# Optimization experiments

Hardware: AMD Instinct MI355X
Metric: run time of the kernel (lower is better)

Reference implementation:

```python
import jax, jax.numpy as jnp
import numpy as np

N_NODES = 50000
NEG_SLOPE = 0.2


def setup_inputs() -> dict:
    key = jax.random.key(0)
    k1, k2, k3, k4, k5 = jax.random.split(key, 5)
    in_c, out_c = 256, 256
    n_edges = 1_600_000
    x = jax.random.normal(k1, (N_NODES, in_c), dtype=jnp.float32)
    edge_index = jax.random.randint(k2, (2, n_edges), 0, N_NODES, dtype=jnp.int64)
    # Glorot-ish scaled params
    W = jax.random.normal(k3, (in_c, out_c), dtype=jnp.float32) * (1.0 / np.sqrt(in_c))
    att_src = jax.random.normal(k4, (out_c,), dtype=jnp.float32) * (1.0 / np.sqrt(out_c))
    att_dst = jax.random.normal(k5, (out_c,), dtype=jnp.float32) * (1.0 / np.sqrt(out_c))
    bias = jnp.zeros((out_c,), dtype=jnp.float32)
    return {"x": x, "edge_index": edge_index, "W": W, "att_src": att_src, "att_dst": att_dst, "bias": bias}


def reference(x, edge_index, W, att_src, att_dst, bias):
    N = x.shape[0]
    # PyG GATConv default: add self loops
    loops = jnp.arange(N, dtype=edge_index.dtype)
    src = jnp.concatenate([edge_index[0], loops])  # [E+N]
    dst = jnp.concatenate([edge_index[1], loops])  # [E+N]

    h = x @ W  # [N, out_c]
    a_s = h @ att_src  # [N] per-node source attention term
    a_d = h @ att_dst  # [N] per-node destination attention term

    e = a_s[src] + a_d[dst]  # [E+N]
    e = jnp.where(e > 0, e, NEG_SLOPE * e)  # LeakyReLU(0.2)

    # scatter-softmax over edges sharing a destination node
    e_max = jax.ops.segment_max(e, dst, num_segments=N)  # [N]
    e_exp = jnp.exp(e - e_max[dst])  # [E+N]
    denom = jax.ops.segment_sum(e_exp, dst, num_segments=N)  # [N]
    alpha = e_exp / denom[dst]  # [E+N]

    msgs = alpha[:, None] * h[src]  # [E+N, out_c]
    out = jax.ops.segment_sum(msgs, dst, num_segments=N)  # [N, out_c]
    return out + bias
```

## Files before the change

kernel.cpp:

```cpp
#include <hip/hip_runtime.h>
#include <math.h>

#define NODES_C 256
#define NEG_SLOPE 0.2f
#define CAP 128
#define NSLICE 8

typedef __attribute__((ext_vector_type(8))) short short8;
typedef __attribute__((ext_vector_type(4))) float f32x4;
typedef __attribute__((ext_vector_type(2))) float f32x2;
typedef __attribute__((ext_vector_type(4))) int i32x4;

__device__ inline unsigned short f2bf(float f) {
    unsigned u = __float_as_uint(f);
    u = (u + 0x7fff + ((u >> 16) & 1)) >> 16;
    return (unsigned short)u;
}
__device__ inline unsigned cvtpk_bf16(float a, float b) {
    unsigned r;
    asm("v_cvt_pk_bf16_f32 %0, %1, %2" : "=v"(r) : "v"(a), "v"(b));
    return r;
}
__device__ inline void gload_lds16(const void* g, void* l) {
    __builtin_amdgcn_global_load_lds(
        (const __attribute__((address_space(1))) unsigned int*)g,
        (__attribute__((address_space(3))) unsigned int*)l, 16, 0, 0);
}
__device__ inline void fma2(f32x2& a, unsigned u, float w) {
    f32x2 h;
    h.x = __uint_as_float(u << 16);
    h.y = __uint_as_float(u & 0xffff0000u);
    a += h * w;
}

__global__ __launch_bounds__(256) void k_init(const float* __restrict__ W,
                                              unsigned short* __restrict__ wt,
                                              uint4* __restrict__ zbase,
                                              int nZero4, int nbZero) {
    const int tid = threadIdx.x;
    int bid = blockIdx.x;
    if (bid < nbZero) {
        const int base = bid * 1024 + tid;
#pragma unroll
        for (int k = 0; k < 4; ++k) {
            const int i = base + k * 256;
            if (i < nZero4) zbase[i] = make_uint4(0, 0, 0, 0);
        }
        return;
    }
    bid -= nbZero;
    const int base = bid * 1024 + tid;
#pragma unroll
    for (int k = 0; k < 4; ++k) {
        const int i = base + k * 256;
        wt[i] = f2bf(W[(i & 255) * NODES_C + (i >> 8)]);
    }
}

__global__ __launch_bounds__(256) void k_stageB(
    const float* __restrict__ x, const unsigned short* __restrict__ wt,
    const float* __restrict__ att_src, const float* __restrict__ att_dst,
    unsigned short* __restrict__ hb, float* __restrict__ a_s, float* __restrict__ a_d,
    int n) {
    __shared__ unsigned short Ab[128 * 32];
    __shared__ unsigned short Bb[128 * 32];
    __shared__ float pfs[2][128], pfd[2][128];
    const int tid = threadIdx.x;
    const int lane = tid & 63;
    const int wid = tid >> 6;

    const int gbid = blockIdx.x;
    const int wr = wid >> 1, wc = wid & 1;
    const int brow = (gbid >> 1) * 128;
    const int bcol = (gbid & 1) * 128;
    const int rsel = lane & 15, ksel = (lane >> 4) * 8;

    f32x4 acc[4][4] = {};
    const int c0 = wid, c1 = wid + 4;
    const int srow0 = c0 * 16 + (lane >> 2), srow1 = c1 * 16 + (lane >> 2);
    const int sk = (lane & 3) * 8;
    const int arow = tid >> 1;
    const int kh = (tid & 1) * 16;
    const float4* xsrc = (const float4*)(x + (size_t)min(brow + arow, n - 1) * NODES_C);
    uint4* adst = (uint4*)&Ab[arow * 32 + kh];

    for (int kk = 0; kk < 256; kk += 32) {
        const int kb = (kk + kh) >> 2;
        const float4 v0 = xsrc[kb + 0];
        const float4 v1 = xsrc[kb + 1];
        const float4 v2 = xsrc[kb + 2];
        const float4 v3 = xsrc[kb + 3];
        gload_lds16(wt + (size_t)(bcol + srow0) * NODES_C + kk + sk, Bb + c0 * 512);
        gload_lds16(wt + (size_t)(bcol + srow1) * NODES_C + kk + sk, Bb + c1 * 512);
        adst[0] = make_uint4(cvtpk_bf16(v0.x, v0.y), cvtpk_bf16(v0.z, v0.w),
                             cvtpk_bf16(v1.x, v1.y), cvtpk_bf16(v1.z, v1.w));
        adst[1] = make_uint4(cvtpk_bf16(v2.x, v2.y), cvtpk_bf16(v2.z, v2.w),
                             cvtpk_bf16(v3.x, v3.y), cvtpk_bf16(v3.z, v3.w));
        __syncthreads();
        short8 afrag[4], bfrag[4];
#pragma unroll
        for (int m = 0; m < 4; ++m)
            afrag[m] = *(const short8*)&Ab[(wr * 64 + m * 16 + rsel) * 32 + ksel];
#pragma unroll
        for (int q = 0; q < 4; ++q)
            bfrag[q] = *(const short8*)&Bb[(wc * 64 + q * 16 + rsel) * 32 + ksel];
#pragma unroll
        for (int m = 0; m < 4; ++m)
#pragma unroll
            for (int q = 0; q < 4; ++q)
                acc[m][q] = __builtin_amdgcn_mfma_f32_16x16x32_bf16(bfrag[q], afrag[m], acc[m][q], 0, 0, 0);
        __syncthreads();
    }

    const int xr = lane & 15;
    const int cg = (lane >> 4) * 4;
    float4 avs4[4], avd4[4];
#pragma unroll
    for (int q = 0; q < 4; ++q) {
        avs4[q] = *(const float4*)&att_src[bcol + wc * 64 + q * 16 + cg];
        avd4[q] = *(const float4*)&att_dst[bcol + wc * 64 + q * 16 + cg];
    }
#pragma unroll
    for (int m = 0; m < 4; ++m) {
        const int rloc = wr * 64 + m * 16 + xr;
        const int r = brow + rloc;
        float s = 0.f, d = 0.f;
#pragma unroll
        for (int q = 0; q < 4; ++q) {
            const f32x4 v = acc[m][q];
            s += v[0] * avs4[q].x + v[1] * avs4[q].y + v[2] * avs4[q].z + v[3] * avs4[q].w;
            d += v[0] * avd4[q].x + v[1] * avd4[q].y + v[2] * avd4[q].z + v[3] * avd4[q].w;
            if (r < n) {
                const uint2 hv = make_uint2(cvtpk_bf16(v[0], v[1]), cvtpk_bf16(v[2], v[3]));
                *(uint2*)&hb[(size_t)r * NODES_C + bcol + wc * 64 + q * 16 + cg] = hv;
            }
        }
        s += __shfl_xor(s, 16); s += __shfl_xor(s, 32);
        d += __shfl_xor(d, 16); d += __shfl_xor(d, 32);
        if (lane < 16) { pfs[wc][rloc] = s; pfd[wc][rloc] = d; }
    }
    __syncthreads();
    if (tid < 128) {
        const int r = brow + tid;
        if (r < n) atomicAdd(&a_s[r], pfs[0][tid] + pfs[1][tid]);
    } else {
        const int t2 = tid - 128;
        const int r = brow + t2;
        if (r < n) atomicAdd(&a_d[r], pfd[0][t2] + pfd[1][t2]);
    }
}

__global__ __launch_bounds__(256) void k_permute(const int* __restrict__ src,
                                                 const int* __restrict__ dst,
                                                 const float* __restrict__ a_s,
                                                 const float* __restrict__ a_d,
                                                 int* __restrict__ cnt,
                                                 unsigned* __restrict__ sedge,
                                                 int E4, int bps, int nsNode, int n) {
    const int slice = blockIdx.x & (NSLICE - 1);
    const int j = blockIdx.x >> 3;
    const int lo = slice * nsNode;
    const int hi = min(lo + nsNode, n);
    const int stride = bps * 256;
    const i32x4* d4 = (const i32x4*)dst;
    const i32x4* s4 = (const i32x4*)src;

    for (int g = j * 256 + threadIdx.x; g < E4; g += stride) {
        const i32x4 dv = __builtin_nontemporal_load(&d4[g]);
        const bool m0 = (dv.x >= lo) & (dv.x < hi);
        const bool m1 = (dv.y >= lo) & (dv.y < hi);
        const bool m2 = (dv.z >= lo) & (dv.z < hi);
        const bool m3 = (dv.w >= lo) & (dv.w < hi);
        if (!(m0 | m1 | m2 | m3)) continue;
        const i32x4 sv = __builtin_nontemporal_load(&s4[g]);
#pragma unroll
        for (int k = 0; k < 4; ++k) {
            const bool mk = k == 0 ? m0 : k == 1 ? m1 : k == 2 ? m2 : m3;
            if (!mk) continue;
            const int d = k == 0 ? dv.x : k == 1 ? dv.y : k == 2 ? dv.z : dv.w;
            const int s = k == 0 ? sv.x : k == 1 ? sv.y : k == 2 ? sv.z : sv.w;
            float e = a_s[s] + a_d[d];
            e = e > 0.f ? e : NEG_SLOPE * e;
            const float w = __expf(e);
            const int pos = atomicAdd(&cnt[d], 1);
            if (pos < CAP) sedge[(d << 7) + pos] = ((unsigned)f2bf(w) << 16) | (unsigned)s;
        }
    }
}

__global__ __launch_bounds__(256) void k_gather(const int* __restrict__ cnt,
                                                const unsigned* __restrict__ sedge,
                                                const unsigned short* __restrict__ hb,
                                                const float* __restrict__ a_s,
                                                const float* __restrict__ a_d,
                                                const float* __restrict__ bias,
                                                float* __restrict__ out, int n) {
    const int node = (int)((blockIdx.x * (size_t)blockDim.x + threadIdx.x) >> 6);
    const int lane = threadIdx.x & 63;
    if (node >= n) return;
    const int c = __builtin_amdgcn_readfirstlane(cnt[node]);
    const int base = node << 7;
    const int hf = lane >> 5, q = lane & 31;
    const uint4* hrow = (const uint4*)hb;

    float eself = a_s[node] + a_d[node];
    eself = eself > 0.f ? eself : NEG_SLOPE * eself;
    const unsigned selfmeta = ((unsigned)f2bf(__expf(eself)) << 16) | (unsigned)node;
    const int items = c + 1;

    f32x2 acc0 = {0.f, 0.f}, acc1 = {0.f, 0.f}, acc2 = {0.f, 0.f}, acc3 = {0.f, 0.f};
    float dsum = 0.f;

    int it = 0;
    for (; it + 16 <= c; it += 16) {
        const int bi = __builtin_amdgcn_readfirstlane(base + it);
        unsigned p[16];
#pragma unroll
        for (int k = 0; k < 16; ++k) p[k] = sedge[bi + k];
        uint4 r[8];
#pragma unroll
        for (int k = 0; k < 8; ++k) {
            const unsigned m = hf ? p[2 * k + 1] : p[2 * k];
            r[k] = hrow[(size_t)(m & 0xffffu) * 32 + q];
        }
#pragma unroll
        for (int k = 0; k < 8; ++k) {
            const unsigned m = hf ? p[2 * k + 1] : p[2 * k];
            const float w = __uint_as_float(m & 0xffff0000u);
            dsum += w;
            fma2(acc0, r[k].x, w); fma2(acc1, r[k].y, w);
            fma2(acc2, r[k].z, w); fma2(acc3, r[k].w, w);
        }
    }
    for (; it < items; it += 2) {
        const int bi = __builtin_amdgcn_readfirstlane(base + it);
        const unsigned m0 = (it     < c) ? sedge[bi]     : ((it     == c) ? selfmeta : 0u);
        const unsigned m1 = (it + 1 < c) ? sedge[bi + 1] : ((it + 1 == c) ? selfmeta : 0u);
        const unsigned m = hf ? m1 : m0;
        const uint4 r = hrow[(size_t)(m & 0xffffu) * 32 + q];
        const float w = __uint_as_float(m & 0xffff0000u);
        dsum += w;
        fma2(acc0, r.x, w); fma2(acc1, r.y, w);
        fma2(acc2, r.z, w); fma2(acc3, r.w, w);
    }

    dsum += __shfl_xor(dsum, 32);
    acc0.x += __shfl_xor(acc0.x, 32); acc0.y += __shfl_xor(acc0.y, 32);
    acc1.x += __shfl_xor(acc1.x, 32); acc1.y += __shfl_xor(acc1.y, 32);
    acc2.x += __shfl_xor(acc2.x, 32); acc2.y += __shfl_xor(acc2.y, 32);
    acc3.x += __shfl_xor(acc3.x, 32); acc3.y += __shfl_xor(acc3.y, 32);

    const float inv = 1.f / dsum;
    const f32x2 A = hf ? acc2 : acc0;
    const f32x2 B = hf ? acc3 : acc1;
    const int ch = q * 8 + hf * 4;
    const float4 b4 = *(const float4*)&bias[ch];
    float4 o;
    o.x = fmaf(A.x, inv, b4.x);
    o.y = fmaf(A.y, inv, b4.y);
    o.z = fmaf(B.x, inv, b4.z);
    o.w = fmaf(B.y, inv, b4.w);
    *(float4*)&out[(size_t)node * NODES_C + ch] = o;
}

extern "C" void kernel_launch(void* const* d_in, const int* in_sizes, int n_in,
                              void* d_out, int out_size, void* d_ws, size_t ws_size,
                              hipStream_t stream) {
    const float* x       = (const float*)d_in[0];
    const int*   edge    = (const int*)d_in[1];
    const float* W       = (const float*)d_in[2];
    const float* att_src = (const float*)d_in[3];
    const float* att_dst = (const float*)d_in[4];
    const float* bias    = (const float*)d_in[5];
    float* out = (float*)d_out;

    const int n = in_sizes[0] / NODES_C;
    const int E = in_sizes[1] / 2;
    const int Mpad = (n + 127) & ~127;
    const int* src = edge;
    const int* dst = edge + E;

    char* p = (char*)d_ws;
    auto carve = [&p](size_t bytes) { char* r = p; p += (bytes + 255) & ~(size_t)255; return r; };
    unsigned short* wt = (unsigned short*)carve((size_t)NODES_C * NODES_C * 2);
    unsigned short* hb = (unsigned short*)carve((size_t)n * NODES_C * 2);
    float* a_s = (float*)carve((size_t)n * 4 * 3);
    float* a_d = a_s + n;
    int*   cnt = (int*)(a_d + n);
    unsigned* sedge = (unsigned*)carve((size_t)n * CAP * 4);

    const int nZero4 = (n * 3) / 4;
    const int nbZero = (nZero4 + 1023) / 1024;
    const int nbCvtw = (NODES_C * NODES_C) / 1024;

    k_init<<<nbZero + nbCvtw, 256, 0, stream>>>(W, wt, (uint4*)a_s, nZero4, nbZero);
    k_stageB<<<(Mpad / 128) * 2, 256, 0, stream>>>(
        x, wt, att_src, att_dst, hb, a_s, a_d, n);

    const int E4 = E / 4;
    const int bps = 192;
    const int nsNode = (n + NSLICE - 1) / NSLICE;
    k_permute<<<bps * NSLICE, 256, 0, stream>>>(src, dst, a_s, a_d, cnt, sedge,
                                                E4, bps, nsNode, n);
    k_gather<<<(n + 3) / 4, 256, 0, stream>>>(cnt, sedge, hb, a_s, a_d, bias, out, n);
}
```

Measured before the change: 236.7 us.

## Precompute attention logits via W·att and co-launch GEMM with edge bucketing

Attention terms a_s/a_d are now computed directly as x·(W·att_src) and x·(W·att_dst) in the init kernel. That removes the epilogue reduction and atomics from the GEMM and lets the edge-bucketing pass run as soon as init finishes. The GEMM and the permute kernel are merged into one launch so their blocks run concurrently, overlapping compute-bound MFMA work with atomic- and memory-bound edge scatter. The gather loop now loads edge metadata as vector uint4 loads and clamps the count to CAP. The cost is an extra fp32 read of x in init and logits computed in fp32 rather than from the bf16-rounded h.

```diff
diff --git a/kernel.cpp b/kernel.cpp
--- a/kernel.cpp
+++ b/kernel.cpp
@@ -5,6 +5,7 @@
 #define NEG_SLOPE 0.2f
 #define CAP 128
 #define NSLICE 8
+#define AROWS 64
 
 typedef __attribute__((ext_vector_type(8))) short short8;
 typedef __attribute__((ext_vector_type(4))) float f32x4;
@@ -33,42 +34,110 @@
     a += h * w;
 }
 
-__global__ __launch_bounds__(256) void k_init(const float* __restrict__ W,
-                                              unsigned short* __restrict__ wt,
-                                              uint4* __restrict__ zbase,
-                                              int nZero4, int nbZero) {
+__global__ __launch_bounds__(256) void k_init(
+    const float* __restrict__ x, const float* __restrict__ W,
+    const float* __restrict__ att_src, const float* __restrict__ att_dst,
+    unsigned short* __restrict__ wt, float* __restrict__ a_s,
+    float* __restrict__ a_d, int* __restrict__ cnt,
+    int n, int nbA, int nbCvtw) {
     const int tid = threadIdx.x;
     int bid = blockIdx.x;
-    if (bid < nbZero) {
+    if (bid < nbA) {
+        __shared__ float vs[NODES_C], vd[NODES_C];
+        {
+            const float4* wr = (const float4*)(W + (size_t)tid * NODES_C);
+            const float4* as4 = (const float4*)att_src;
+            const float4* ad4 = (const float4*)att_dst;
+            float s = 0.f, d = 0.f;
+            for (int c = 0; c < NODES_C / 4; ++c) {
+                const float4 wv = wr[c], av = as4[c], bv = ad4[c];
+                s += wv.x * av.x + wv.y * av.y + wv.z * av.z + wv.w * av.w;
+                d += wv.x * bv.x + wv.y * bv.y + wv.z * bv.z + wv.w * bv.w;
+            }
+            vs[tid] = s; vd[tid] = d;
+        }
+        __syncthreads();
+        const int lane = tid & 63, wid = tid >> 6;
+        const float4 vsl = ((const float4*)vs)[lane];
+        const float4 vdl = ((const float4*)vd)[lane];
+        const int rend = min(bid * AROWS + AROWS, n);
+        for (int r = bid * AROWS + wid; r < rend; r += 4) {
+            const float4 xv = ((const float4*)(x + (size_t)r * NODES_C))[lane];
+            float s = xv.x * vsl.x + xv.y * vsl.y + xv.z * vsl.z + xv.w * vsl.w;
+            float d = xv.x * vdl.x + xv.y * vdl.y + xv.z * vdl.z + xv.w * vdl.w;
+#pragma unroll
+            for (int off = 32; off; off >>= 1) {
+                s += __shfl_xor(s, off);
+                d += __shfl_xor(d, off);
+            }
+            if (lane == 0) { a_s[r] = s; a_d[r] = d; }
+        }
+        return;
+    }
+    bid -= nbA;
+    if (bid < nbCvtw) {
         const int base = bid * 1024 + tid;
 #pragma unroll
         for (int k = 0; k < 4; ++k) {
             const int i = base + k * 256;
-            if (i < nZero4) zbase[i] = make_uint4(0, 0, 0, 0);
+            wt[i] = f2bf(W[(i & 255) * NODES_C + (i >> 8)]);
         }
         return;
     }
-    bid -= nbZero;
+    bid -= nbCvtw;
     const int base = bid * 1024 + tid;
 #pragma unroll
     for (int k = 0; k < 4; ++k) {
         const int i = base + k * 256;
-        wt[i] = f2bf(W[(i & 255) * NODES_C + (i >> 8)]);
-    }
-}
-
-__global__ __launch_bounds__(256) void k_stageB(
+        if (i < n) cnt[i] = 0;
+    }
+}
+
+__global__ __launch_bounds__(256) void k_fat(
     const float* __restrict__ x, const unsigned short* __restrict__ wt,
-    const float* __restrict__ att_src, const float* __restrict__ att_dst,
-    unsigned short* __restrict__ hb, float* __restrict__ a_s, float* __restrict__ a_d,
-    int n) {
+    unsigned short* __restrict__ hb,
+    const int* __restrict__ src, const int* __restrict__ dst,
+    const float* __restrict__ a_s, const float* __restrict__ a_d,
+    int* __restrict__ cnt, unsigned* __restrict__ sedge,
+    int n, int nbG, int E4, int bps, int nsNode) {
     __shared__ unsigned short Ab[128 * 32];
     __shared__ unsigned short Bb[128 * 32];
-    __shared__ float pfs[2][128], pfd[2][128];
     const int tid = threadIdx.x;
+
+    if (blockIdx.x >= nbG) {
+        const int slice = blockIdx.x & (NSLICE - 1);
+        const int j = (blockIdx.x - nbG) >> 3;
+        const int lo = slice * nsNode;
+        const int hi = min(lo + nsNode, n);
+        const int stride = bps * 256;
+        const i32x4* d4 = (const i32x4*)dst;
+        const i32x4* s4 = (const i32x4*)src;
+        for (int g = j * 256 + tid; g < E4; g += stride) {
+            const i32x4 dv = __builtin_nontemporal_load(&d4[g]);
+            const bool m0 = (dv.x >= lo) & (dv.x < hi);
+            const bool m1 = (dv.y >= lo) & (dv.y < hi);
+            const bool m2 = (dv.z >= lo) & (dv.z < hi);
+            const bool m3 = (dv.w >= lo) & (dv.w < hi);
+            if (!(m0 | m1 | m2 | m3)) continue;
+            const i32x4 sv = __builtin_nontemporal_load(&s4[g]);
+#pragma unroll
+            for (int k = 0; k < 4; ++k) {
+                const bool mk = k == 0 ? m0 : k == 1 ? m1 : k == 2 ? m2 : m3;
+                if (!mk) continue;
+                const int d = k == 0 ? dv.x : k == 1 ? dv.y : k == 2 ? dv.z : dv.w;
+                const int s = k == 0 ? sv.x : k == 1 ? sv.y : k == 2 ? sv.z : sv.w;
+                float e = a_s[s] + a_d[d];
+                e = e > 0.f ? e : NEG_SLOPE * e;
+                const float w = __expf(e);
+                const int pos = atomicAdd(&cnt[d], 1);
+                if (pos < CAP) sedge[(d << 7) + pos] = ((unsigned)f2bf(w) << 16) | (unsigned)s;
+            }
+        }
+        return;
+    }
+
     const int lane = tid & 63;
     const int wid = tid >> 6;
-
     const int gbid = blockIdx.x;
     const int wr = wid >> 1, wc = wid & 1;
     const int brow = (gbid >> 1) * 128;
@@ -114,76 +183,16 @@
 
     const int xr = lane & 15;
     const int cg = (lane >> 4) * 4;
-    float4 avs4[4], avd4[4];
-#pragma unroll
-    for (int q = 0; q < 4; ++q) {
-        avs4[q] = *(const float4*)&att_src[bcol + wc * 64 + q * 16 + cg];
-        avd4[q] = *(const float4*)&att_dst[bcol + wc * 64 + q * 16 + cg];
-    }
 #pragma unroll
     for (int m = 0; m < 4; ++m) {
-        const int rloc = wr * 64 + m * 16 + xr;
-        const int r = brow + rloc;
-        float s = 0.f, d = 0.f;
-#pragma unroll
-        for (int q = 0; q < 4; ++q) {
-            const f32x4 v = acc[m][q];
-            s += v[0] * avs4[q].x + v[1] * avs4[q].y + v[2] * avs4[q].z + v[3] * avs4[q].w;
-            d += v[0] * avd4[q].x + v[1] * avd4[q].y + v[2] * avd4[q].z + v[3] * avd4[q].w;
-            if (r < n) {
+        const int r = brow + wr * 64 + m * 16 + xr;
+        if (r < n) {
+#pragma unroll
+            for (int q = 0; q < 4; ++q) {
+                const f32x4 v = acc[m][q];
                 const uint2 hv = make_uint2(cvtpk_bf16(v[0], v[1]), cvtpk_bf16(v[2], v[3]));
                 *(uint2*)&hb[(size_t)r * NODES_C + bcol + wc * 64 + q * 16 + cg] = hv;
             }
-        }
-        s += __shfl_xor(s, 16); s += __shfl_xor(s, 32);
-        d += __shfl_xor(d, 16); d += __shfl_xor(d, 32);
-        if (lane < 16) { pfs[wc][rloc] = s; pfd[wc][rloc] = d; }
-    }
-    __syncthreads();
-    if (tid < 128) {
-        const int r = brow + tid;
-        if (r < n) atomicAdd(&a_s[r], pfs[0][tid] + pfs[1][tid]);
-    } else {
-        const int t2 = tid - 128;
-        const int r = brow + t2;
-        if (r < n) atomicAdd(&a_d[r], pfd[0][t2] + pfd[1][t2]);
-    }
-}
-
-__global__ __launch_bounds__(256) void k_permute(const int* __restrict__ src,
-                                                 const int* __restrict__ dst,
-                                                 const float* __restrict__ a_s,
-                                                 const float* __restrict__ a_d,
-                                                 int* __restrict__ cnt,
-                                                 unsigned* __restrict__ sedge,
-                                                 int E4, int bps, int nsNode, int n) {
-    const int slice = blockIdx.x & (NSLICE - 1);
-    const int j = blockIdx.x >> 3;
-    const int lo = slice * nsNode;
-    const int hi = min(lo + nsNode, n);
-    const int stride = bps * 256;
-    const i32x4* d4 = (const i32x4*)dst;
-    const i32x4* s4 = (const i32x4*)src;
-
-    for (int g = j * 256 + threadIdx.x; g < E4; g += stride) {
-        const i32x4 dv = __builtin_nontemporal_load(&d4[g]);
-        const bool m0 = (dv.x >= lo) & (dv.x < hi);
-        const bool m1 = (dv.y >= lo) & (dv.y < hi);
-        const bool m2 = (dv.z >= lo) & (dv.z < hi);
-        const bool m3 = (dv.w >= lo) & (dv.w < hi);
-        if (!(m0 | m1 | m2 | m3)) continue;
-        const i32x4 sv = __builtin_nontemporal_load(&s4[g]);
-#pragma unroll
-        for (int k = 0; k < 4; ++k) {
-            const bool mk = k == 0 ? m0 : k == 1 ? m1 : k == 2 ? m2 : m3;
-            if (!mk) continue;
-            const int d = k == 0 ? dv.x : k == 1 ? dv.y : k == 2 ? dv.z : dv.w;
-            const int s = k == 0 ? sv.x : k == 1 ? sv.y : k == 2 ? sv.z : sv.w;
-            float e = a_s[s] + a_d[d];
-            e = e > 0.f ? e : NEG_SLOPE * e;
-            const float w = __expf(e);
-            const int pos = atomicAdd(&cnt[d], 1);
-            if (pos < CAP) sedge[(d << 7) + pos] = ((unsigned)f2bf(w) << 16) | (unsigned)s;
         }
     }
 }
@@ -198,7 +207,7 @@
     const int node = (int)((blockIdx.x * (size_t)blockDim.x + threadIdx.x) >> 6);
     const int lane = threadIdx.x & 63;
     if (node >= n) return;
-    const int c = __builtin_amdgcn_readfirstlane(cnt[node]);
+    const int c = min(__builtin_amdgcn_readfirstlane(cnt[node]), CAP);
     const int base = node << 7;
     const int hf = lane >> 5, q = lane & 31;
     const uint4* hrow = (const uint4*)hb;
@@ -214,29 +223,49 @@
     int it = 0;
     for (; it + 16 <= c; it += 16) {
         const int bi = __builtin_amdgcn_readfirstlane(base + it);
-        unsigned p[16];
-#pragma unroll
-        for (int k = 0; k < 16; ++k) p[k] = sedge[bi + k];
-        uint4 r[8];
-#pragma unroll
-        for (int k = 0; k < 8; ++k) {
-            const unsigned m = hf ? p[2 * k + 1] : p[2 * k];
-            r[k] = hrow[(size_t)(m & 0xffffu) * 32 + q];
-        }
-#pragma unroll
-        for (int k = 0; k < 8; ++k) {
-            const unsigned m = hf ? p[2 * k + 1] : p[2 * k];
-            const float w = __uint_as_float(m & 0xffff0000u);
-            dsum += w;
-            fma2(acc0, r[k].x, w); fma2(acc1, r[k].y, w);
-            fma2(acc2, r[k].z, w); fma2(acc3, r[k].w, w);
-        }
+        const uint4 pA = *(const uint4*)&sedge[bi];
+        const uint4 pB = *(const uint4*)&sedge[bi + 4];
+        const uint4 pC = *(const uint4*)&sedge[bi + 8];
+        const uint4 pD = *(const uint4*)&sedge[bi + 12];
+        const unsigned m0 = hf ? pA.y : pA.x;
+        const unsigned m1 = hf ? pA.w : pA.z;
+        const unsigned m2 = hf ? pB.y : pB.x;
+        const unsigned m3 = hf ? pB.w : pB.z;
+        const unsigned m4 = hf ? pC.y : pC.x;
+        const unsigned m5 = hf ? pC.w : pC.z;
+        const unsigned m6 = hf ? pD.y : pD.x;
+        const unsigned m7 = hf ? pD.w : pD.z;
+        const uint4 r0 = hrow[(size_t)(m0 & 0xffffu) * 32 + q];
+        const uint4 r1 = hrow[(size_t)(m1 & 0xffffu) * 32 + q];
+        const uint4 r2 = hrow[(size_t)(m2 & 0xffffu) * 32 + q];
+        const uint4 r3 = hrow[(size_t)(m3 & 0xffffu) * 32 + q];
+        const uint4 r4 = hrow[(size_t)(m4 & 0xffffu) * 32 + q];
+        const uint4 r5 = hrow[(size_t)(m5 & 0xffffu) * 32 + q];
+        const uint4 r6 = hrow[(size_t)(m6 & 0xffffu) * 32 + q];
+        const uint4 r7 = hrow[(size_t)(m7 & 0xffffu) * 32 + q];
+        float w;
+        w = __uint_as_float(m0 & 0xffff0000u); dsum += w;
+        fma2(acc0, r0.x, w); fma2(acc1, r0.y, w); fma2(acc2, r0.z, w); fma2(acc3, r0.w, w);
+        w = __uint_as_float(m1 & 0xffff0000u); dsum += w;
+        fma2(acc0, r1.x, w); fma2(acc1, r1.y, w); fma2(acc2, r1.z, w); fma2(acc3, r1.w, w);
+        w = __uint_as_float(m2 & 0xffff0000u); dsum += w;
+        fma2(acc0, r2.x, w); fma2(acc1, r2.y, w); fma2(acc2, r2.z, w); fma2(acc3, r2.w, w);
+        w = __uint_as_float(m3 & 0xffff0000u); dsum += w;
+        fma2(acc0, r3.x, w); fma2(acc1, r3.y, w); fma2(acc2, r3.z, w); fma2(acc3, r3.w, w);
+        w = __uint_as_float(m4 & 0xffff0000u); dsum += w;
+        fma2(acc0, r4.x, w); fma2(acc1, r4.y, w); fma2(acc2, r4.z, w); fma2(acc3, r4.w, w);
+        w = __uint_as_float(m5 & 0xffff0000u); dsum += w;
+        fma2(acc0, r5.x, w); fma2(acc1, r5.y, w); fma2(acc2, r5.z, w); fma2(acc3, r5.w, w);
+        w = __uint_as_float(m6 & 0xffff0000u); dsum += w;
+        fma2(acc0, r6.x, w); fma2(acc1, r6.y, w); fma2(acc2, r6.z, w); fma2(acc3, r6.w, w);
+        w = __uint_as_float(m7 & 0xffff0000u); dsum += w;
+        fma2(acc0, r7.x, w); fma2(acc1, r7.y, w); fma2(acc2, r7.z, w); fma2(acc3, r7.w, w);
     }
     for (; it < items; it += 2) {
         const int bi = __builtin_amdgcn_readfirstlane(base + it);
-        const unsigned m0 = (it     < c) ? sedge[bi]     : ((it     == c) ? selfmeta : 0u);
-        const unsigned m1 = (it + 1 < c) ? sedge[bi + 1] : ((it + 1 == c) ? selfmeta : 0u);
-        const unsigned m = hf ? m1 : m0;
+        const unsigned t0 = (it     < c) ? sedge[bi]     : ((it     == c) ? selfmeta : 0u);
+        const unsigned t1 = (it + 1 < c) ? sedge[bi + 1] : ((it + 1 == c) ? selfmeta : 0u);
+        const unsigned m = hf ? t1 : t0;
         const uint4 r = hrow[(size_t)(m & 0xffffu) * 32 + q];
         const float w = __uint_as_float(m & 0xffff0000u);
         dsum += w;
@@ -284,23 +313,24 @@
     auto carve = [&p](size_t bytes) { char* r = p; p += (bytes + 255) & ~(size_t)255; return r; };
     unsigned short* wt = (unsigned short*)carve((size_t)NODES_C * NODES_C * 2);
     unsigned short* hb = (unsigned short*)carve((size_t)n * NODES_C * 2);
-    float* a_s = (float*)carve((size_t)n * 4 * 3);
-    float* a_d = a_s + n;
-    int*   cnt = (int*)(a_d + n);
+    float* a_s = (float*)carve((size_t)n * 4);
+    float* a_d = (float*)carve((size_t)n * 4);
+    int*   cnt = (int*)carve((size_t)n * 4);
     unsigned* sedge = (unsigned*)carve((size_t)n * CAP * 4);
 
-    const int nZero4 = (n * 3) / 4;
-    const int nbZero = (nZero4 + 1023) / 1024;
+    const int nbA    = (n + AROWS - 1) / AROWS;
     const int nbCvtw = (NODES_C * NODES_C) / 1024;
-
-    k_init<<<nbZero + nbCvtw, 256, 0, stream>>>(W, wt, (uint4*)a_s, nZero4, nbZero);
-    k_stageB<<<(Mpad / 128) * 2, 256, 0, stream>>>(
-        x, wt, att_src, att_dst, hb, a_s, a_d, n);
-
+    const int nbZ    = (n + 1023) / 1024;
+
+    k_init<<<nbA + nbCvtw + nbZ, 256, 0, stream>>>(
+        x, W, att_src, att_dst, wt, a_s, a_d, cnt, n, nbA, nbCvtw);
+
+    const int nbG = (Mpad / 128) * 2;
     const int E4 = E / 4;
     const int bps = 192;
     const int nsNode = (n + NSLICE - 1) / NSLICE;
-    k_permute<<<bps * NSLICE, 256, 0, stream>>>(src, dst, a_s, a_d, cnt, sedge,
-                                                E4, bps, nsNode, n);
+    k_fat<<<nbG + bps * NSLICE, 256, 0, stream>>>(
+        x, wt, hb, src, dst, a_s, a_d, cnt, sedge, n, nbG, E4, bps, nsNode);
+
     k_gather<<<(n + 3) / 4, 256, 0, stream>>>(cnt, sedge, hb, a_s, a_d, bias, out, n);
 }
```

Result: slower. 275.9 us (+16.5%).
